# Performance work log

Measured on AMD Instinct MI355X. Metric: run time of the kernel, lower is better.

The kernel has to match this reference:

```python
import jax, jax.numpy as jnp
import numpy as np

NUM_SITES = 64
PHYS_DIM = 2
BOND_DIM = 32
BATCH = 65536


def _build_mps(num_sites, phys_dim, bond_dim, seed=0):
    """Replicates ImprovedMPS._initialize_tensors + _canonical_form, then
    zero-pads ragged cores into a dense [S, D, p, D] stack."""
    rng = np.random.default_rng(seed)
    tensors = []
    cur = 1
    for i in range(num_sites):
        if i == 0:
            nb = min(bond_dim, phys_dim)
            shape = (1, phys_dim, nb)
            cur = nb
        elif i == num_sites - 1:
            shape = (cur, phys_dim, 1)
        else:
            nb = min(bond_dim, cur * phys_dim)
            shape = (cur, phys_dim, nb)
            cur = nb
        ld, rd = shape[0] * shape[1], shape[2]
        m = (rng.standard_normal((ld, rd)) * 0.1).astype(np.float32)
        if ld >= rd:
            q, _ = np.linalg.qr(m)
            t = q.reshape(shape)
        else:
            q, _ = np.linalg.qr(m.T)
            t = q.T.reshape(shape)
        tensors.append(t.astype(np.float32))
    # left-canonical sweep
    for i in range(num_sites - 1):
        l, p, r = tensors[i].shape
        q, rr = np.linalg.qr(tensors[i].reshape(l * p, r))
        tensors[i] = q.reshape(l, p, q.shape[1]).astype(np.float32)
        nl, npd, nr = tensors[i + 1].shape
        tensors[i + 1] = (rr @ tensors[i + 1].reshape(nl, npd * nr)).reshape(rr.shape[0], npd, nr).astype(np.float32)
    # zero-pad ragged bonds into dense stack [S, D, p, D]
    A = np.zeros((num_sites, bond_dim, phys_dim, bond_dim), dtype=np.float32)
    for i, t in enumerate(tensors):
        l, p, r = t.shape
        A[i, :l, :, :r] = t
    return A


def setup_inputs() -> dict:
    key = jax.random.key(0)
    x_batch = jax.random.normal(key, (BATCH, NUM_SITES, PHYS_DIM), dtype=jnp.float32)
    A = jnp.asarray(_build_mps(NUM_SITES, PHYS_DIM, BOND_DIM))
    return {"x_batch": x_batch, "A": A}


def reference(x_batch, A):
    # x_batch: [B, S, p]; A: [S, D, p, D] (zero-padded ragged MPS cores)
    B = x_batch.shape[0]
    D = A.shape[1]
    # left_vector starts as ones(B,1) in the ragged view == one-hot e0 in padded view
    left0 = jnp.zeros((B, D), dtype=x_batch.dtype).at[:, 0].set(1.0)
    xs = jnp.moveaxis(x_batch, 1, 0)  # [S, B, p]

    def step(left, inp):
        A_i, x_i = inp  # [D, p, D], [B, p]
        # fuses: contracted = einsum('bp,lpd->bld'); left = einsum('bl,bld->bd')
        left = jnp.einsum('bl,bp,lpd->bd', left, x_i, A_i)
        return left, None

    left, _ = jax.lax.scan(step, left0, (A, xs))
    return left[:, :1]  # last core has right bond 1 -> only col 0 is nonzero
```

## Files before the change

### kernel.cpp

```cpp
#include <hip/hip_runtime.h>


typedef _Float16 half8 __attribute__((ext_vector_type(8)));
typedef _Float16 half4 __attribute__((ext_vector_type(4)));
typedef float floatx16 __attribute__((ext_vector_type(16)));
typedef float f32x4 __attribute__((ext_vector_type(4)));

#define NPAIRS 32
#define GCH 8192
#define XSTRIDE 129

__global__ void mps_prep_pair(const float* __restrict__ A, _Float16* __restrict__ Gf) {
    __shared__ float sA[1024];
    __shared__ float sB[1024];
    __shared__ float sG[1024];
    const int blk = blockIdx.x;
    const int P   = blk >> 2;
    const int pq  = blk & 3;
    const int p   = pq >> 1, q = pq & 1;
    const int tid = threadIdx.x;
    const int row = tid >> 3;
    const int c4  = (tid & 7) * 4;

    *(f32x4*)&sA[row * 32 + c4] =
        *(const f32x4*)(A + ((size_t)(2 * P) * 32 + row) * 64 + p * 32 + c4);
    *(f32x4*)&sB[row * 32 + c4] =
        *(const f32x4*)(A + ((size_t)(2 * P + 1) * 32 + row) * 64 + q * 32 + c4);
    __syncthreads();
    {
        f32x4 acc;
        acc[0] = 0.f; acc[1] = 0.f; acc[2] = 0.f; acc[3] = 0.f;
        for (int m = 0; m < 32; ++m) {
            const float av = sA[row * 32 + m];
            const f32x4 bv = *(const f32x4*)&sB[m * 32 + c4];
            acc[0] += av * bv[0]; acc[1] += av * bv[1];
            acc[2] += av * bv[2]; acc[3] += av * bv[3];
        }
        *(f32x4*)&sG[row * 32 + c4] = acc;
    }
    __syncthreads();
    if (tid < 128) {
        const int lh   = tid >> 6;
        const int lane = tid & 63;
        const int h    = lane >> 5;
        const int d    = lane & 31;
        half8 v;
#pragma unroll
        for (int e = 0; e < 8; ++e) {
            const int l = 16 * lh + (e & 3) + 8 * (e >> 2) + 4 * h;
            v[e] = (_Float16)sG[l * 32 + d];
        }
        reinterpret_cast<half8*>(Gf)[((size_t)P * 8 + pq * 2 + lh) * 64 + lane] = v;
    }
}

#define MF32(A_, B_, C_) __builtin_amdgcn_mfma_f32_32x32x16_f16(A_, B_, C_, 0, 0, 0)

__global__ __launch_bounds__(256, 2) void mps_main(const float* __restrict__ x,
                                                   const _Float16* __restrict__ Gf,
                                                   float* __restrict__ out) {
    __shared__ __align__(16) _Float16 smG[2 * GCH];
    __shared__ __align__(8)  half4    smX[32 * XSTRIDE];

    const int tid  = threadIdx.x;
    const int lane = tid & 63;
    const int wid  = tid >> 6;
    const int brow = blockIdx.x * 128;
    const int col  = lane & 31;
    const int r    = wid * 32 + col;

#pragma unroll
    for (int r_ = 0; r_ < 4; ++r_) {
        const int rec = r_ * 4 + wid;
        const _Float16* g = Gf + rec * 512 + lane * 8;
        __builtin_amdgcn_global_load_lds(
            (const __attribute__((address_space(1))) void*)g,
            (__attribute__((address_space(3))) void*)&smG[rec * 512],
            16, 0, 0);
    }

#pragma unroll
    for (int i = 0; i < 16; ++i) {
        const int j   = i * 256 + tid;
        const int row = j >> 5, q = j & 31;
        const f32x4 v = *(const f32x4*)(x + (size_t)(brow + row) * 128 + 4 * q);
        half4 hv;
        hv[0] = (_Float16)v[0]; hv[1] = (_Float16)v[1];
        hv[2] = (_Float16)v[2]; hv[3] = (_Float16)v[3];
        smX[q * XSTRIDE + row] = hv;
    }

    floatx16 zv;
#pragma unroll
    for (int i = 0; i < 16; ++i) zv[i] = 0.f;

    floatx16 acc;
#pragma unroll
    for (int i = 0; i < 16; ++i) acc[i] = 0.f;
    if (lane < 32) acc[0] = 1.f;

    __syncthreads();

#pragma unroll 1
    for (int C = 0; C < 16; ++C) {
        const int buf = C & 1;
        if (C < 15) {
            const int nbuf = buf ^ 1;
#pragma unroll
            for (int r_ = 0; r_ < 4; ++r_) {
                const int rec = r_ * 4 + wid;
                const _Float16* g = Gf + (size_t)(C + 1) * GCH + rec * 512 + lane * 8;
                __builtin_amdgcn_global_load_lds(
                    (const __attribute__((address_space(1))) void*)g,
                    (__attribute__((address_space(3))) void*)&smG[nbuf * GCH + rec * 512],
                    16, 0, 0);
            }
        }
#pragma unroll
        for (int LP = 0; LP < 2; ++LP) {
            const int P = 2 * C + LP;
            const half4 xq = smX[P * XSTRIDE + r];
            const _Float16 w00 = xq[0] * xq[2];
            const _Float16 w01 = xq[0] * xq[3];
            const _Float16 w10 = xq[1] * xq[2];
            const _Float16 w11 = xq[1] * xq[3];
            half8 G0, G1, G2, G3, G4, G5, G6, G7;
            {
                const _Float16* gb = &smG[buf * GCH + LP * 8 * 512 + lane * 8];
                G0 = *(const half8*)(gb + 0 * 512);
                G1 = *(const half8*)(gb + 1 * 512);
                G2 = *(const half8*)(gb + 2 * 512);
                G3 = *(const half8*)(gb + 3 * 512);
                G4 = *(const half8*)(gb + 4 * 512);
                G5 = *(const half8*)(gb + 5 * 512);
                G6 = *(const half8*)(gb + 6 * 512);
                G7 = *(const half8*)(gb + 7 * 512);
            }
            half8 FA0, FA1;
#pragma unroll
            for (int i_ = 0; i_ < 8; ++i_) {
                FA0[i_] = (_Float16)acc[i_];
                FA1[i_] = (_Float16)acc[8 + i_];
            }
            floatx16 t;
            t = MF32(G0, FA0 * w00, zv);
            t = MF32(G1, FA1 * w00, t);
            t = MF32(G2, FA0 * w01, t);
            t = MF32(G3, FA1 * w01, t);
            t = MF32(G4, FA0 * w10, t);
            t = MF32(G5, FA1 * w10, t);
            t = MF32(G6, FA0 * w11, t);
            t = MF32(G7, FA1 * w11, t);
            acc = t;
        }
        __syncthreads();
    }

    if (lane < 32) out[brow + wid * 32 + lane] = acc[0];
}

extern "C" void kernel_launch(void* const* d_in, const int* in_sizes, int n_in,
                              void* d_out, int out_size, void* d_ws, size_t ws_size,
                              hipStream_t stream) {
    const float* x = (const float*)d_in[0];
    const float* A = (const float*)d_in[1];
    float* outp = (float*)d_out;
    _Float16* Gf = (_Float16*)d_ws;

    hipLaunchKernelGGL(mps_prep_pair, dim3(NPAIRS * 4), dim3(256), 0, stream, A, Gf);
    hipLaunchKernelGGL(mps_main, dim3(65536 / 128), dim3(256), 0, stream, x, Gf, outp);
}
```

Before: 29.86 us.

## Split MPS chain into left and right halves contracted concurrently then dot

The prep kernel now also writes transposed pair-cores for a right-to-left sweep. The main kernel runs 8 waves per block: four contract sites 0-31 from the left and four contract sites 63-32 from the right, each doing 16 pair steps instead of 32. The two 32-wide boundary vectors are combined with a dot product through LDS at the end. This halves the serial dependency chain per batch row, at the cost of twice the waves per block, extra LDS traffic and a final reduction.

```diff
diff --git a/kernel.cpp b/kernel.cpp
--- a/kernel.cpp
+++ b/kernel.cpp
@@ -7,8 +7,9 @@
 typedef float f32x4 __attribute__((ext_vector_type(4)));
 
 #define NPAIRS 32
-#define GCH 8192
+#define GSTEP 8192
 #define XSTRIDE 129
+#define GF2_OFS 131072
 
 __global__ void mps_prep_pair(const float* __restrict__ A, _Float16* __restrict__ Gf) {
     __shared__ float sA[1024];
@@ -39,11 +40,11 @@
         *(f32x4*)&sG[row * 32 + c4] = acc;
     }
     __syncthreads();
+    const int lane = tid & 63;
+    const int h    = lane >> 5;
     if (tid < 128) {
-        const int lh   = tid >> 6;
-        const int lane = tid & 63;
-        const int h    = lane >> 5;
-        const int d    = lane & 31;
+        const int lh = tid >> 6;
+        const int d  = lane & 31;
         half8 v;
 #pragma unroll
         for (int e = 0; e < 8; ++e) {
@@ -51,37 +52,54 @@
             v[e] = (_Float16)sG[l * 32 + d];
         }
         reinterpret_cast<half8*>(Gf)[((size_t)P * 8 + pq * 2 + lh) * 64 + lane] = v;
+    } else {
+        const int dh = (tid >> 6) & 1;
+        const int l  = lane & 31;
+        const int j  = 31 - P;
+        half8 v;
+#pragma unroll
+        for (int e = 0; e < 8; ++e) {
+            const int d = 16 * dh + (e & 3) + 8 * (e >> 2) + 4 * h;
+            v[e] = (_Float16)sG[l * 32 + d];
+        }
+        reinterpret_cast<half8*>(Gf + GF2_OFS)[((size_t)j * 8 + pq * 2 + dh) * 64 + lane] = v;
     }
 }
 
 #define MF32(A_, B_, C_) __builtin_amdgcn_mfma_f32_32x32x16_f16(A_, B_, C_, 0, 0, 0)
 
-__global__ __launch_bounds__(256, 2) void mps_main(const float* __restrict__ x,
+__global__ __launch_bounds__(512, 2) void mps_main(const float* __restrict__ x,
                                                    const _Float16* __restrict__ Gf,
                                                    float* __restrict__ out) {
-    __shared__ __align__(16) _Float16 smG[2 * GCH];
+    __shared__ __align__(16) _Float16 smG[2 * GSTEP];
     __shared__ __align__(8)  half4    smX[32 * XSTRIDE];
 
     const int tid  = threadIdx.x;
     const int lane = tid & 63;
     const int wid  = tid >> 6;
+    const int w4   = wid & 3;
+    const int is_b = wid >> 2;
     const int brow = blockIdx.x * 128;
     const int col  = lane & 31;
-    const int r    = wid * 32 + col;
-
-#pragma unroll
-    for (int r_ = 0; r_ < 4; ++r_) {
-        const int rec = r_ * 4 + wid;
-        const _Float16* g = Gf + rec * 512 + lane * 8;
+    const int h    = lane >> 5;
+    const int r    = w4 * 32 + col;
+
+    const _Float16* GfB = Gf + GF2_OFS;
+
+    {
+        const _Float16* gA = Gf + wid * 512 + lane * 8;
         __builtin_amdgcn_global_load_lds(
-            (const __attribute__((address_space(1))) void*)g,
-            (__attribute__((address_space(3))) void*)&smG[rec * 512],
-            16, 0, 0);
-    }
-
-#pragma unroll
-    for (int i = 0; i < 16; ++i) {
-        const int j   = i * 256 + tid;
+            (const __attribute__((address_space(1))) void*)gA,
+            (__attribute__((address_space(3))) void*)&smG[wid * 512], 16, 0, 0);
+        const _Float16* gB = GfB + wid * 512 + lane * 8;
+        __builtin_amdgcn_global_load_lds(
+            (const __attribute__((address_space(1))) void*)gB,
+            (__attribute__((address_space(3))) void*)&smG[4096 + wid * 512], 16, 0, 0);
+    }
+
+#pragma unroll
+    for (int i = 0; i < 8; ++i) {
+        const int j   = i * 512 + tid;
         const int row = j >> 5, q = j & 31;
         const f32x4 v = *(const f32x4*)(x + (size_t)(brow + row) * 128 + 4 * q);
         half4 hv;
@@ -102,40 +120,37 @@
     __syncthreads();
 
 #pragma unroll 1
-    for (int C = 0; C < 16; ++C) {
-        const int buf = C & 1;
-        if (C < 15) {
+    for (int s = 0; s < 16; ++s) {
+        const int buf = s & 1;
+        if (s < 15) {
             const int nbuf = buf ^ 1;
-#pragma unroll
-            for (int r_ = 0; r_ < 4; ++r_) {
-                const int rec = r_ * 4 + wid;
-                const _Float16* g = Gf + (size_t)(C + 1) * GCH + rec * 512 + lane * 8;
-                __builtin_amdgcn_global_load_lds(
-                    (const __attribute__((address_space(1))) void*)g,
-                    (__attribute__((address_space(3))) void*)&smG[nbuf * GCH + rec * 512],
-                    16, 0, 0);
-            }
-        }
-#pragma unroll
-        for (int LP = 0; LP < 2; ++LP) {
-            const int P = 2 * C + LP;
-            const half4 xq = smX[P * XSTRIDE + r];
+            const _Float16* gA = Gf + (size_t)(s + 1) * 4096 + wid * 512 + lane * 8;
+            __builtin_amdgcn_global_load_lds(
+                (const __attribute__((address_space(1))) void*)gA,
+                (__attribute__((address_space(3))) void*)&smG[nbuf * GSTEP + wid * 512],
+                16, 0, 0);
+            const _Float16* gB = GfB + (size_t)(s + 1) * 4096 + wid * 512 + lane * 8;
+            __builtin_amdgcn_global_load_lds(
+                (const __attribute__((address_space(1))) void*)gB,
+                (__attribute__((address_space(3))) void*)&smG[nbuf * GSTEP + 4096 + wid * 512],
+                16, 0, 0);
+        }
+        {
+            const int qidx = is_b ? (31 - s) : s;
+            const half4 xq = smX[qidx * XSTRIDE + r];
             const _Float16 w00 = xq[0] * xq[2];
             const _Float16 w01 = xq[0] * xq[3];
             const _Float16 w10 = xq[1] * xq[2];
             const _Float16 w11 = xq[1] * xq[3];
-            half8 G0, G1, G2, G3, G4, G5, G6, G7;
-            {
-                const _Float16* gb = &smG[buf * GCH + LP * 8 * 512 + lane * 8];
-                G0 = *(const half8*)(gb + 0 * 512);
-                G1 = *(const half8*)(gb + 1 * 512);
-                G2 = *(const half8*)(gb + 2 * 512);
-                G3 = *(const half8*)(gb + 3 * 512);
-                G4 = *(const half8*)(gb + 4 * 512);
-                G5 = *(const half8*)(gb + 5 * 512);
-                G6 = *(const half8*)(gb + 6 * 512);
-                G7 = *(const half8*)(gb + 7 * 512);
-            }
+            const _Float16* gb = &smG[buf * GSTEP + is_b * 4096 + lane * 8];
+            const half8 G0 = *(const half8*)(gb + 0 * 512);
+            const half8 G1 = *(const half8*)(gb + 1 * 512);
+            const half8 G2 = *(const half8*)(gb + 2 * 512);
+            const half8 G3 = *(const half8*)(gb + 3 * 512);
+            const half8 G4 = *(const half8*)(gb + 4 * 512);
+            const half8 G5 = *(const half8*)(gb + 5 * 512);
+            const half8 G6 = *(const half8*)(gb + 6 * 512);
+            const half8 G7 = *(const half8*)(gb + 7 * 512);
             half8 FA0, FA1;
 #pragma unroll
             for (int i_ = 0; i_ < 8; ++i_) {
@@ -156,7 +171,23 @@
         __syncthreads();
     }
 
-    if (lane < 32) out[brow + wid * 32 + lane] = acc[0];
+    {
+        float* uvb = (float*)smG;
+        const int vofs = is_b * 4096;
+#pragma unroll
+        for (int reg = 0; reg < 16; ++reg) {
+            const int li = (reg & 3) + 8 * (reg >> 2) + 4 * h;
+            uvb[vofs + li * 128 + r] = acc[reg];
+        }
+        __syncthreads();
+        if (tid < 128) {
+            float sum = 0.f;
+#pragma unroll
+            for (int li = 0; li < 32; ++li)
+                sum += uvb[li * 128 + tid] * uvb[4096 + li * 128 + tid];
+            out[brow + tid] = sum;
+        }
+    }
 }
 
 extern "C" void kernel_launch(void* const* d_in, const int* in_sizes, int n_in,
@@ -168,5 +199,5 @@
     _Float16* Gf = (_Float16*)d_ws;
 
     hipLaunchKernelGGL(mps_prep_pair, dim3(NPAIRS * 4), dim3(256), 0, stream, A, Gf);
-    hipLaunchKernelGGL(mps_main, dim3(65536 / 128), dim3(256), 0, stream, x, Gf, outp);
+    hipLaunchKernelGGL(mps_main, dim3(65536 / 128), dim3(512), 0, stream, x, Gf, outp);
 }
```

Result: no change. 30.33 us (+1.6%).
